# Kernel optimization log

Hardware: AMD Instinct MI355X
Metric: run time of the kernel (lower is better)

Reference implementation:

```python
import jax, jax.numpy as jnp
import numpy as np

HEADS, DH, M_LAND, PINV_ITERS, LN_EPS = 8, 64, 256, 6, 1e-5


def layer_norm(x, g, b):
    mu = x.mean(-1, keepdims=True)
    var = ((x - mu) ** 2).mean(-1, keepdims=True)
    return (x - mu) * jax.lax.rsqrt(var + LN_EPS) * g + b


def moore_penrose_pinv(x, iters=PINV_ITERS):
    # x: (h, m, m). Iterative Newton-Schulz style pinv (lucidrains).
    abs_x = jnp.abs(x)
    col = abs_x.sum(-1)
    row = abs_x.sum(-2)
    z = jnp.swapaxes(x, -1, -2) / (jnp.max(col) * jnp.max(row))
    I = jnp.eye(x.shape[-1], dtype=x.dtype)
    for _ in range(iters):
        xz = x @ z
        z = 0.25 * z @ (13.0 * I - xz @ (15.0 * I - xz @ (7.0 * I - xz)))
    return z


def nystrom_attention(x, qkv_w, out_w, out_b, res_w):
    # x: (n, dim). No mask, eval mode (dropout off).
    n, dim = x.shape
    pad = (-n) % M_LAND
    xp = jnp.pad(x, ((pad, 0), (0, 0)))  # pad at sequence START, as in original
    n_p = n + pad
    l = n_p // M_LAND  # tokens per landmark
    qkv = xp @ qkv_w  # (n_p, 3*h*dh)
    q, k, v = jnp.split(qkv, 3, axis=-1)
    split = lambda t: t.reshape(n_p, HEADS, DH).transpose(1, 0, 2)  # (h, n_p, dh)
    q, k, v = split(q), split(k), split(v)
    q = q * (DH ** -0.5)
    q_l = q.reshape(HEADS, M_LAND, l, DH).mean(axis=2)  # (h, m, dh)
    k_l = k.reshape(HEADS, M_LAND, l, DH).mean(axis=2)
    sim1 = jnp.einsum('hid,hjd->hij', q, k_l)    # (h, n_p, m)
    sim2 = jnp.einsum('hid,hjd->hij', q_l, k_l)  # (h, m, m)
    sim3 = jnp.einsum('hid,hjd->hij', q_l, k)    # (h, m, n_p)
    a1 = jax.nn.softmax(sim1, axis=-1)
    a2 = jax.nn.softmax(sim2, axis=-1)
    a3 = jax.nn.softmax(sim3, axis=-1)
    a2_inv = moore_penrose_pinv(a2)
    out = a1 @ (a2_inv @ (a3 @ v))  # (h, n_p, dh)
    # residual depthwise conv over sequence dim, kernel 33, per head
    res = jax.lax.conv_general_dilated(
        v[None], res_w, (1, 1), ((16, 16), (0, 0)),
        feature_group_count=HEADS, dimension_numbers=('NCHW', 'OIHW', 'NCHW'))[0]
    out = out + res
    out = out.transpose(1, 0, 2).reshape(n_p, HEADS * DH)
    out = out @ out_w + out_b
    return out[-n:]  # drop the leading pad


def ppeg(x, w7, b7, w5, b5, w3, b3, H, W):
    cls_tok, feat = x[0], x[1:]
    C = feat.shape[1]
    img = feat.T.reshape(1, C, H, W)
    def dw(w, b, p):
        y = jax.lax.conv_general_dilated(
            img, w, (1, 1), ((p, p), (p, p)),
            feature_group_count=C, dimension_numbers=('NCHW', 'OIHW', 'NCHW'))
        return y + b.reshape(1, C, 1, 1)
    out = img + dw(w7, b7, 3) + dw(w5, b5, 2) + dw(w3, b3, 1)
    out = out[0].reshape(C, H * W).T
    return jnp.concatenate([cls_tok[None], out], axis=0)


def forward(h, fc1_w, fc1_b, cls_token, l1_ln_g, l1_ln_b, l1_qkv_w, l1_out_w, l1_out_b, l1_res_w,
            conv7_w, conv7_b, conv5_w, conv5_b, conv3_w, conv3_b,
            l2_ln_g, l2_ln_b, l2_qkv_w, l2_out_w, l2_out_b, l2_res_w,
            norm_g, norm_b, fc2_w, fc2_b):
    x = jax.nn.relu(h @ fc1_w + fc1_b)  # (N, 512)
    N = x.shape[0]
    Hs = Ws = int(np.ceil(np.sqrt(N)))  # N chosen perfect square -> add_length == 0
    x = jnp.concatenate([cls_token, x], axis=0)  # (N+1, 512)
    x = x + nystrom_attention(layer_norm(x, l1_ln_g, l1_ln_b), l1_qkv_w, l1_out_w, l1_out_b, l1_res_w)
    x = ppeg(x, conv7_w, conv7_b, conv5_w, conv5_b, conv3_w, conv3_b, Hs, Ws)
    x = x + nystrom_attention(layer_norm(x, l2_ln_g, l2_ln_b), l2_qkv_w, l2_out_w, l2_out_b, l2_res_w)
    x = layer_norm(x, norm_g, norm_b)[0]  # cls token readout
    return x @ fc2_w + fc2_b  # (n_classes,)


def setup_inputs() -> dict:
    key = jax.random.key(0)
    ks = jax.random.split(key, 16)
    nrm = lambda k, s, sc=0.02: jax.random.normal(k, s, jnp.float32) * sc
    D = 512
    return {
        'h': jax.random.normal(ks[0], (16384, 2048), jnp.float32),
        'fc1_w': nrm(ks[1], (2048, D)), 'fc1_b': jnp.zeros((D,), jnp.float32),
        'cls_token': nrm(ks[2], (1, D), 1.0),
        'l1_ln_g': jnp.ones((D,), jnp.float32), 'l1_ln_b': jnp.zeros((D,), jnp.float32),
        'l1_qkv_w': nrm(ks[3], (D, 3 * D)),
        'l1_out_w': nrm(ks[4], (D, D)), 'l1_out_b': jnp.zeros((D,), jnp.float32),
        'l1_res_w': nrm(ks[5], (HEADS, 1, 33, 1), 0.05),
        'conv7_w': nrm(ks[6], (D, 1, 7, 7), 0.05), 'conv7_b': jnp.zeros((D,), jnp.float32),
        'conv5_w': nrm(ks[7], (D, 1, 5, 5), 0.05), 'conv5_b': jnp.zeros((D,), jnp.float32),
        'conv3_w': nrm(ks[8], (D, 1, 3, 3), 0.05), 'conv3_b': jnp.zeros((D,), jnp.float32),
        'l2_ln_g': jnp.ones((D,), jnp.float32), 'l2_ln_b': jnp.zeros((D,), jnp.float32),
        'l2_qkv_w': nrm(ks[9], (D, 3 * D)),
        'l2_out_w': nrm(ks[10], (D, D)), 'l2_out_b': jnp.zeros((D,), jnp.float32),
        'l2_res_w': nrm(ks[11], (HEADS, 1, 33, 1), 0.05),
        'norm_g': jnp.ones((D,), jnp.float32), 'norm_b': jnp.zeros((D,), jnp.float32),
        'fc2_w': nrm(ks[12], (D, 2)), 'fc2_b': jnp.zeros((2,), jnp.float32),
    }


def reference(h, fc1_w, fc1_b, cls_token, l1_ln_g, l1_ln_b, l1_qkv_w, l1_out_w, l1_out_b, l1_res_w,
              conv7_w, conv7_b, conv5_w, conv5_b, conv3_w, conv3_b,
              l2_ln_g, l2_ln_b, l2_qkv_w, l2_out_w, l2_out_b, l2_res_w,
              norm_g, norm_b, fc2_w, fc2_b):
    return forward(h, fc1_w, fc1_b, cls_token, l1_ln_g, l1_ln_b, l1_qkv_w, l1_out_w, l1_out_b, l1_res_w,
                   conv7_w, conv7_b, conv5_w, conv5_b, conv3_w, conv3_b,
                   l2_ln_g, l2_ln_b, l2_qkv_w, l2_out_w, l2_out_b, l2_res_w,
                   norm_g, norm_b, fc2_w, fc2_b)
```

## Files before the change

### kernel.cpp

```cpp
#include <hip/hip_runtime.h>
#include <cstddef>

#define NROWS 16385
#define NPAD  16640
#define PADT  255
#define DIM   512
#define HEADS 8
#define DH    64
#define NL    256
#define LCH   65
#define LCHUNK 65
#define SLACK 24
#define LDST  40
#define AST   72

typedef short bf16x8 __attribute__((ext_vector_type(8)));
typedef float f32x4  __attribute__((ext_vector_type(4)));

__device__ __forceinline__ float wsum(float v){
#pragma unroll
  for (int o = 32; o; o >>= 1) v += __shfl_xor(v, o);
  return v;
}
__device__ __forceinline__ float wmax(float v){
#pragma unroll
  for (int o = 32; o; o >>= 1) v = fmaxf(v, __shfl_xor(v, o));
  return v;
}

__device__ __forceinline__ void split2(float x, unsigned short &h, unsigned short &l){
  unsigned ux = __float_as_uint(x);
  unsigned rh = (ux + 0x7FFFu + ((ux >> 16) & 1u)) >> 16;
  h = (unsigned short)rh;
  float fh = __uint_as_float(rh << 16);
  float r = x - fh;
  unsigned ur = __float_as_uint(r);
  unsigned rl = (ur + 0x7FFFu + ((ur >> 16) & 1u)) >> 16;
  l = (unsigned short)rl;
}
__device__ __forceinline__ float bf2f(unsigned short h){
  return __uint_as_float((unsigned)h << 16);
}

__global__ __launch_bounds__(256) void gemm64_sp_kernel(
    const unsigned short* __restrict__ Ah, const unsigned short* __restrict__ Al,
    const unsigned short* __restrict__ Bth, const unsigned short* __restrict__ Btl,
    const unsigned short* __restrict__ IBh, const unsigned short* __restrict__ IBl,
    float* __restrict__ Cf,
    unsigned short* __restrict__ Crh, unsigned short* __restrict__ Crl,
    unsigned short* __restrict__ Cth, unsigned short* __restrict__ Ctl,
    int M, int N, int K, long sA, long sB, long sC,
    float alpha, float ib)
{
  size_t zo = (size_t)blockIdx.z;
  Ah  += zo*sA; Al  += zo*sA;
  Bth += zo*sB; Btl += zo*sB;
  if (IBh){ IBh += zo*sA; IBl += zo*sA; }
  if (Cf)  Cf  += zo*sC;
  if (Crh){ Crh += zo*sC; Crl += zo*sC; }
  if (Cth){ Cth += zo*sC; Ctl += zo*sC; }
  __shared__ unsigned short LAh[64*LDST], LAl[64*LDST], LBh[64*LDST], LBl[64*LDST];
  const int t = threadIdx.x;
  const int wid = t >> 6, lane = t & 63;
  const int wr = wid >> 1, wc = wid & 1;
  const int l15 = lane & 15, kb = lane >> 4;
  const int bm = blockIdx.y << 6, bn = blockIdx.x << 6;
  const int r4 = t >> 2, kc = (t & 3) << 3;
  f32x4 acc[2][2];
#pragma unroll
  for (int i=0;i<2;++i)
#pragma unroll
    for (int j=0;j<2;++j) acc[i][j] = (f32x4){0.f,0.f,0.f,0.f};

  for (int k0 = 0; k0 < K; k0 += 32){
    __syncthreads();
    {
      int lo = r4*LDST + kc;
      *(uint4*)&LAh[lo] = *(const uint4*)&Ah[(size_t)(bm+r4)*K + k0 + kc];
      *(uint4*)&LAl[lo] = *(const uint4*)&Al[(size_t)(bm+r4)*K + k0 + kc];
      *(uint4*)&LBh[lo] = *(const uint4*)&Bth[(size_t)(bn+r4)*K + k0 + kc];
      *(uint4*)&LBl[lo] = *(const uint4*)&Btl[(size_t)(bn+r4)*K + k0 + kc];
    }
    __syncthreads();
    bf16x8 ah[2], al[2], bh[2], bl[2];
#pragma unroll
    for (int r=0;r<2;++r){
      int off = (wr*32 + r*16 + l15)*LDST + kb*8;
      ah[r] = *(const bf16x8*)&LAh[off];
      al[r] = *(const bf16x8*)&LAl[off];
    }
#pragma unroll
    for (int c2=0;c2<2;++c2){
      int off = (wc*32 + c2*16 + l15)*LDST + kb*8;
      bh[c2] = *(const bf16x8*)&LBh[off];
      bl[c2] = *(const bf16x8*)&LBl[off];
    }
#pragma unroll
    for (int r=0;r<2;++r)
#pragma unroll
      for (int c2=0;c2<2;++c2){
        acc[r][c2] = __builtin_amdgcn_mfma_f32_16x16x32_bf16(ah[r], bh[c2], acc[r][c2], 0,0,0);
        acc[r][c2] = __builtin_amdgcn_mfma_f32_16x16x32_bf16(ah[r], bl[c2], acc[r][c2], 0,0,0);
        acc[r][c2] = __builtin_amdgcn_mfma_f32_16x16x32_bf16(al[r], bh[c2], acc[r][c2], 0,0,0);
      }
  }
#pragma unroll
  for (int r=0;r<2;++r){
#pragma unroll
    for (int c2=0;c2<2;++c2){
      int col = bn + wc*32 + c2*16 + l15;
      int rb  = bm + wr*32 + r*16 + kb*4;
      float v[4];
#pragma unroll
      for (int e=0;e<4;++e){
        float x = acc[r][c2][e];
        if (ib != 0.f){
          size_t io = (size_t)(rb+e)*K + col;
          float ibv = bf2f(IBh[io]) + bf2f(IBl[io]);
          x = alpha*(ib*ibv - x);
        } else {
          x = alpha*x;
        }
        v[e] = x;
      }
      if (Cf){
#pragma unroll
        for (int e=0;e<4;++e) Cf[(size_t)(rb+e)*N + col] = v[e];
      }
      if (Crh){
#pragma unroll
        for (int e=0;e<4;++e){
          unsigned short hh, ll;
          split2(v[e], hh, ll);
          Crh[(size_t)(rb+e)*N + col] = hh;
          Crl[(size_t)(rb+e)*N + col] = ll;
        }
      }
      if (Cth){
        unsigned short h4[4], l4[4];
#pragma unroll
        for (int e=0;e<4;++e) split2(v[e], h4[e], l4[e]);
        uint2 uh, ul;
        uh.x = (unsigned)h4[0] | ((unsigned)h4[1]<<16);
        uh.y = (unsigned)h4[2] | ((unsigned)h4[3]<<16);
        ul.x = (unsigned)l4[0] | ((unsigned)l4[1]<<16);
        ul.y = (unsigned)l4[2] | ((unsigned)l4[3]<<16);
        *(uint2*)&Cth[(size_t)col*M + rb] = uh;
        *(uint2*)&Ctl[(size_t)col*M + rb] = ul;
      }
    }
  }
}

__global__ __launch_bounds__(256) void gemm_sb_kernel(
    const unsigned short* __restrict__ Ah, const unsigned short* __restrict__ Al,
    const unsigned short* __restrict__ BTh, const unsigned short* __restrict__ BTl,
    const float* __restrict__ bias, float* __restrict__ C,
    int M, int N, int K, int accum)
{
  __shared__ unsigned short LAh[128*LDST], LAl[128*LDST], LBh[128*LDST], LBl[128*LDST];
  const int t = threadIdx.x;
  const int bm = blockIdx.y << 7, bn = blockIdx.x << 7;
  const int wid = t >> 6, lane = t & 63;
  const int wr = wid >> 1, wc = wid & 1;
  const int l15 = lane & 15, kb = lane >> 4;
  const int sr = t >> 1, sc0 = (t & 1) << 4;
  f32x4 acc[4][4];
#pragma unroll
  for (int i=0;i<4;++i)
#pragma unroll
    for (int j=0;j<4;++j) acc[i][j] = (f32x4){0.f,0.f,0.f,0.f};

  const uint4 zz = make_uint4(0,0,0,0);
  for (int k0 = 0; k0 < K; k0 += 32){
    __syncthreads();
    {
      bool av = (bm + sr) < M;
      size_t ga = (size_t)(bm + sr)*K + k0 + sc0;
      uint4 a0 = av ? *(const uint4*)(Ah + ga)     : zz;
      uint4 a1 = av ? *(const uint4*)(Ah + ga + 8) : zz;
      uint4 a2 = av ? *(const uint4*)(Al + ga)     : zz;
      uint4 a3 = av ? *(const uint4*)(Al + ga + 8) : zz;
      size_t gb = (size_t)(bn + sr)*K + k0 + sc0;
      uint4 b0 = *(const uint4*)(BTh + gb);
      uint4 b1 = *(const uint4*)(BTh + gb + 8);
      uint4 b2 = *(const uint4*)(BTl + gb);
      uint4 b3 = *(const uint4*)(BTl + gb + 8);
      int lo = sr*LDST + sc0;
      *(uint4*)&LAh[lo] = a0; *(uint4*)&LAh[lo+8] = a1;
      *(uint4*)&LAl[lo] = a2; *(uint4*)&LAl[lo+8] = a3;
      *(uint4*)&LBh[lo] = b0; *(uint4*)&LBh[lo+8] = b1;
      *(uint4*)&LBl[lo] = b2; *(uint4*)&LBl[lo+8] = b3;
    }
    __syncthreads();
    bf16x8 ah[4], al[4], bh[4], bl[4];
#pragma unroll
    for (int ai=0; ai<4; ++ai){
      int off = (wr*64 + ai*16 + l15)*LDST + kb*8;
      ah[ai] = *(const bf16x8*)&LAh[off];
      al[ai] = *(const bf16x8*)&LAl[off];
    }
#pragma unroll
    for (int bj=0; bj<4; ++bj){
      int off = (wc*64 + bj*16 + l15)*LDST + kb*8;
      bh[bj] = *(const bf16x8*)&LBh[off];
      bl[bj] = *(const bf16x8*)&LBl[off];
    }
#pragma unroll
    for (int ai=0; ai<4; ++ai)
#pragma unroll
      for (int bj=0; bj<4; ++bj){
        acc[ai][bj] = __builtin_amdgcn_mfma_f32_16x16x32_bf16(ah[ai], bh[bj], acc[ai][bj], 0,0,0);
        acc[ai][bj] = __builtin_amdgcn_mfma_f32_16x16x32_bf16(ah[ai], bl[bj], acc[ai][bj], 0,0,0);
        acc[ai][bj] = __builtin_amdgcn_mfma_f32_16x16x32_bf16(al[ai], bh[bj], acc[ai][bj], 0,0,0);
      }
  }
#pragma unroll
  for (int ai=0; ai<4; ++ai){
#pragma unroll
    for (int bj=0; bj<4; ++bj){
      int col = bn + wc*64 + bj*16 + l15;
      float bv = bias ? bias[col] : 0.f;
#pragma unroll
      for (int r=0; r<4; ++r){
        int row = bm + wr*64 + ai*16 + kb*4 + r;
        if (row < M){
          float v = acc[ai][bj][r] + bv;
          if (accum) v += C[(size_t)row*N + col];
          C[(size_t)row*N + col] = v;
        }
      }
    }
  }
}

__global__ __launch_bounds__(256) void gemm_sbf_kernel(
    const float* __restrict__ A,
    const unsigned short* __restrict__ BTh, const unsigned short* __restrict__ BTl,
    const float* __restrict__ bias, float* __restrict__ C,
    int M, int N, int K, int relu)
{
  __shared__ unsigned short LAh[128*LDST], LAl[128*LDST], LBh[128*LDST], LBl[128*LDST];
  const int t = threadIdx.x;
  const int bm = blockIdx.y << 7, bn = blockIdx.x << 7;
  const int wid = t >> 6, lane = t & 63;
  const int wr = wid >> 1, wc = wid & 1;
  const int l15 = lane & 15, kb = lane >> 4;
  const int sr = t >> 1, sc0 = (t & 1) << 4;
  f32x4 acc[4][4];
#pragma unroll
  for (int i=0;i<4;++i)
#pragma unroll
    for (int j=0;j<4;++j) acc[i][j] = (f32x4){0.f,0.f,0.f,0.f};

  for (int k0 = 0; k0 < K; k0 += 32){
    __syncthreads();
    {
      const float* ap = A + (size_t)(bm + sr)*K + k0 + sc0;
      float va[16];
      *(float4*)&va[0]  = ((const float4*)ap)[0];
      *(float4*)&va[4]  = ((const float4*)ap)[1];
      *(float4*)&va[8]  = ((const float4*)ap)[2];
      *(float4*)&va[12] = ((const float4*)ap)[3];
      int lo = sr*LDST + sc0;
      unsigned* dh = (unsigned*)&LAh[lo];
      unsigned* dl = (unsigned*)&LAl[lo];
#pragma unroll
      for (int q=0;q<8;++q){
        unsigned short h0,l0,h1,l1;
        split2(va[2*q],   h0, l0);
        split2(va[2*q+1], h1, l1);
        dh[q] = (unsigned)h0 | ((unsigned)h1 << 16);
        dl[q] = (unsigned)l0 | ((unsigned)l1 << 16);
      }
      size_t gb = (size_t)(bn + sr)*K + k0 + sc0;
      uint4 b0 = *(const uint4*)(BTh + gb);
      uint4 b1 = *(const uint4*)(BTh + gb + 8);
      uint4 b2 = *(const uint4*)(BTl + gb);
      uint4 b3 = *(const uint4*)(BTl + gb + 8);
      *(uint4*)&LBh[lo] = b0; *(uint4*)&LBh[lo+8] = b1;
      *(uint4*)&LBl[lo] = b2; *(uint4*)&LBl[lo+8] = b3;
    }
    __syncthreads();
    bf16x8 ah[4], al[4], bh[4], bl[4];
#pragma unroll
    for (int ai=0; ai<4; ++ai){
      int off = (wr*64 + ai*16 + l15)*LDST + kb*8;
      ah[ai] = *(const bf16x8*)&LAh[off];
      al[ai] = *(const bf16x8*)&LAl[off];
    }
#pragma unroll
    for (int bj=0; bj<4; ++bj){
      int off = (wc*64 + bj*16 + l15)*LDST + kb*8;
      bh[bj] = *(const bf16x8*)&LBh[off];
      bl[bj] = *(const bf16x8*)&LBl[off];
    }
#pragma unroll
    for (int ai=0; ai<4; ++ai)
#pragma unroll
      for (int bj=0; bj<4; ++bj){
        acc[ai][bj] = __builtin_amdgcn_mfma_f32_16x16x32_bf16(ah[ai], bh[bj], acc[ai][bj], 0,0,0);
        acc[ai][bj] = __builtin_amdgcn_mfma_f32_16x16x32_bf16(ah[ai], bl[bj], acc[ai][bj], 0,0,0);
        acc[ai][bj] = __builtin_amdgcn_mfma_f32_16x16x32_bf16(al[ai], bh[bj], acc[ai][bj], 0,0,0);
      }
  }
#pragma unroll
  for (int ai=0; ai<4; ++ai){
#pragma unroll
    for (int bj=0; bj<4; ++bj){
      int col = bn + wc*64 + bj*16 + l15;
      float bv = bias ? bias[col] : 0.f;
#pragma unroll
      for (int r=0; r<4; ++r){
        int row = bm + wr*64 + ai*16 + kb*4 + r;
        float v = acc[ai][bj][r] + bv;
        if (relu) v = fmaxf(v, 0.f);
        C[(size_t)row*N + col] = v;
      }
    }
  }
}

__global__ void wt_split_T_kernel(const float* __restrict__ W,
                                  unsigned short* __restrict__ BTh,
                                  unsigned short* __restrict__ BTl, int K, int N)
{
  int idx = blockIdx.x*256 + threadIdx.x;
  if (idx >= N*K) return;
  int n = idx / K, k = idx - n*K;
  unsigned short h, l;
  split2(W[(size_t)k*N + n], h, l);
  BTh[idx] = h; BTl[idx] = l;
}

__global__ void att_split_kernel(const float* __restrict__ ATT,
                                 unsigned short* __restrict__ Ah,
                                 unsigned short* __restrict__ Al)
{
  size_t i4 = (size_t)blockIdx.x*256 + threadIdx.x;
  size_t e = i4*4;
  int row = (int)(e >> 9);
  float4 v = make_float4(0.f,0.f,0.f,0.f);
  if (row < NROWS) v = *(const float4*)(ATT + (size_t)PADT*DIM + e);
  unsigned short h0,l0,h1,l1,h2,l2,h3,l3;
  split2(v.x,h0,l0); split2(v.y,h1,l1); split2(v.z,h2,l2); split2(v.w,h3,l3);
  uint2 uh, ul;
  uh.x = (unsigned)h0 | ((unsigned)h1<<16); uh.y = (unsigned)h2 | ((unsigned)h3<<16);
  ul.x = (unsigned)l0 | ((unsigned)l1<<16); ul.y = (unsigned)l2 | ((unsigned)l3<<16);
  *(uint2*)(Ah + e) = uh;
  *(uint2*)(Al + e) = ul;
}

__global__ __launch_bounds__(256) void ln_pad_sb_kernel(
    const float* __restrict__ X, const float* __restrict__ g,
    const float* __restrict__ b, unsigned short* __restrict__ Yh,
    unsigned short* __restrict__ Yl)
{
  int p = blockIdx.x;
  int t = threadIdx.x;
  size_t base = (size_t)p*DIM;
  if (p < PADT){
    Yh[base+t] = 0; Yh[base+t+256] = 0;
    Yl[base+t] = 0; Yl[base+t+256] = 0;
    return;
  }
  const float* xr = X + (size_t)(p-PADT)*DIM;
  float x0 = xr[t], x1 = xr[t+256];
  float s = x0 + x1, sq = x0*x0 + x1*x1;
  s = wsum(s); sq = wsum(sq);
  __shared__ float rs[4], rq[4];
  if ((t&63)==0){ rs[t>>6]=s; rq[t>>6]=sq; }
  __syncthreads();
  float S = rs[0]+rs[1]+rs[2]+rs[3];
  float SQ = rq[0]+rq[1]+rq[2]+rq[3];
  float mu = S * (1.f/DIM);
  float var = SQ * (1.f/DIM) - mu*mu;
  float r = rsqrtf(var + 1e-5f);
  float y0 = (x0-mu)*r*g[t]     + b[t];
  float y1 = (x1-mu)*r*g[t+256] + b[t+256];
  unsigned short h, l;
  split2(y0, h, l); Yh[base+t] = h;     Yl[base+t] = l;
  split2(y1, h, l); Yh[base+t+256] = h; Yl[base+t+256] = l;
}

__global__ void landmarks_kernel(const float* __restrict__ QKV,
                                 float* __restrict__ QL, float* __restrict__ KL)
{
  int m = blockIdx.x, h = blockIdx.y, d = threadIdx.x;
  float sq = 0.f, sk = 0.f;
  const float* base = QKV + (size_t)(m*LCH)*1536 + (h<<6) + d;
  for (int j = 0; j < LCH; ++j){
    sq += base[0];
    sk += base[512];
    base += 1536;
  }
  QL[(((h<<8)+m)<<6) + d] = sq * (0.125f/65.f);
  KL[(((h<<8)+m)<<6) + d] = sk * (1.f/65.f);
}

__global__ void klsplit_kernel(const float* __restrict__ KL,
                               unsigned short* __restrict__ KLh,
                               unsigned short* __restrict__ KLl)
{
  int i = blockIdx.x*256 + threadIdx.x;
  unsigned short h, l;
  split2(KL[i], h, l);
  KLh[i] = h; KLl[i] = l;
}

__global__ __launch_bounds__(256) void sim2_kernel(
    const float* __restrict__ QL, const float* __restrict__ KL, float* __restrict__ A2)
{
  int m = blockIdx.x, h = blockIdx.y, n = threadIdx.x;
  __shared__ float ql[64];
  __shared__ float red[4];
  if (n < 64) ql[n] = QL[(((h<<8)+m)<<6) + n];
  __syncthreads();
  const float* kl = KL + (size_t)(((h<<8)+n)<<6);
  float s = 0.f;
#pragma unroll
  for (int d=0; d<64; ++d) s += ql[d]*kl[d];
  float mx = wmax(s);
  if ((n&63)==0) red[n>>6] = mx;
  __syncthreads();
  mx = fmaxf(fmaxf(red[0],red[1]), fmaxf(red[2],red[3]));
  float e = __expf(s - mx);
  float sm = wsum(e);
  __syncthreads();
  if ((n&63)==0) red[n>>6] = sm;
  __syncthreads();
  sm = red[0]+red[1]+red[2]+red[3];
  A2[((size_t)((h<<8)+m)<<8) + n] = e/sm;
}

__global__ void crsum_kernel(const float* __restrict__ A2, float* __restrict__ CR)
{
  int b = blockIdx.x, t = threadIdx.x;
  float v;
  if (b < 2048){
    v = fabsf(A2[((size_t)b<<8) + t]);
  } else {
    int r = b - 2048;
    int h = r >> 8, n = r & 255;
    v = fabsf(A2[((size_t)h<<16) + (t<<8) + n]);
  }
  v = wsum(v);
  __shared__ float red[4];
  if ((t&63)==0) red[t>>6]=v;
  __syncthreads();
  if (t==0) CR[b] = red[0]+red[1]+red[2]+red[3];
}
__global__ void maxprod_kernel(const float* __restrict__ CR, float* __restrict__ SCAL)
{
  int t = threadIdx.x;
  float mc = -3e38f, mr = -3e38f;
  for (int i=t; i<2048; i+=256){ mc = fmaxf(mc, CR[i]); mr = fmaxf(mr, CR[2048+i]); }
  mc = wmax(mc); mr = wmax(mr);
  __shared__ float rc[4], rr[4];
  if ((t&63)==0){ rc[t>>6]=mc; rr[t>>6]=mr; }
  __syncthreads();
  if (t==0){
    float a = fmaxf(fmaxf(rc[0],rc[1]),fmaxf(rc[2],rc[3]));
    float b = fmaxf(fmaxf(rr[0],rr[1]),fmaxf(rr[2],rr[3]));
    SCAL[0] = 1.f/(a*b);
  }
}

__global__ void tsplit_kernel(const float* __restrict__ A2, const float* __restrict__ SCAL,
                              unsigned short* __restrict__ A2h, unsigned short* __restrict__ A2l,
                              unsigned short* __restrict__ Zrh, unsigned short* __restrict__ Zrl,
                              unsigned short* __restrict__ Zth, unsigned short* __restrict__ Ztl)
{
  int idx = blockIdx.x*256 + threadIdx.x;
  int h = idx >> 16, rem = idx & 65535, m = rem >> 8, n = rem & 255;
  float a = A2[idx];
  unsigned short hh, ll;
  split2(a, hh, ll);
  A2h[idx] = hh; A2l[idx] = ll;
  float z = a * SCAL[0];
  split2(z, hh, ll);
  Zth[idx] = hh; Ztl[idx] = ll;
  size_t rmo = ((size_t)h<<16) + (n<<8) + m;
  Zrh[rmo] = hh; Zrl[rmo] = ll;
}

__global__ __launch_bounds__(256) void lattn3_kernel(
    const float* __restrict__ QKV, const float* __restrict__ QL,
    float* __restrict__ PACC, float* __restrict__ PML)
{
  const int c = blockIdx.x, lg = blockIdx.y, h = blockIdx.z;
  const int t = threadIdx.x;
  const int w = t >> 6, lane = t & 63;
  const int l15 = lane & 15, kb = lane >> 4;
  __shared__ unsigned short LQh[64*AST], LQl[64*AST];
  __shared__ unsigned short LKh[64*AST], LKl[64*AST];
  __shared__ unsigned short LPh[64*AST], LPl[64*AST];
  const int sr = t >> 2, sc0 = (t & 3) << 4;
  {
    const float* qp = QL + (((size_t)(h*256 + lg*64 + sr)) << 6) + sc0;
    float va[16];
    *(float4*)&va[0]  = ((const float4*)qp)[0];
    *(float4*)&va[4]  = ((const float4*)qp)[1];
    *(float4*)&va[8]  = ((const float4*)qp)[2];
    *(float4*)&va[12] = ((const float4*)qp)[3];
    unsigned* dh = (unsigned*)&LQh[sr*AST + sc0];
    unsigned* dl = (unsigned*)&LQl[sr*AST + sc0];
#pragma unroll
    for (int q=0;q<8;++q){
      unsigned short h0,l0,h1,l1;
      split2(va[2*q],   h0, l0);
      split2(va[2*q+1], h1, l1);
      dh[q] = (unsigned)h0 | ((unsigned)h1 << 16);
      dl[q] = (unsigned)l0 | ((unsigned)l1 << 16);
    }
  }
  float m = -3e38f, l = 0.f;
  f32x4 oacc[4];
#pragma unroll
  for (int i=0;i<4;++i) oacc[i] = (f32x4){0.f,0.f,0.f,0.f};

  for (int s = 0; s < 4; ++s){
    const int kbase = c*256 + s*64;
    __syncthreads();
    {
      const float* kp = QKV + (size_t)(kbase + sr)*1536 + 512 + (h<<6) + sc0;
      float va[16];
      *(float4*)&va[0]  = ((const float4*)kp)[0];
      *(float4*)&va[4]  = ((const float4*)kp)[1];
      *(float4*)&va[8]  = ((const float4*)kp)[2];
      *(float4*)&va[12] = ((const float4*)kp)[3];
      unsigned* dh = (unsigned*)&LKh[sr*AST + sc0];
      unsigned* dl = (unsigned*)&LKl[sr*AST + sc0];
#pragma unroll
      for (int q=0;q<8;++q){
        unsigned short h0,l0,h1,l1;
        split2(va[2*q],   h0, l0);
        split2(va[2*q+1], h1, l1);
        dh[q] = (unsigned)h0 | ((unsigned)h1 << 16);
        dl[q] = (unsigned)l0 | ((unsigned)l1 << 16);
      }
    }
    __syncthreads();
    f32x4 sacc[4];
#pragma unroll
    for (int i=0;i<4;++i) sacc[i] = (f32x4){0.f,0.f,0.f,0.f};
#pragma unroll
    for (int ks = 0; ks < 2; ++ks){
      int qoff = (w*16 + l15)*AST + ks*32 + kb*8;
      bf16x8 bh = *(const bf16x8*)&LQh[qoff];
      bf16x8 bl = *(const bf16x8*)&LQl[qoff];
#pragma unroll
      for (int mi=0; mi<4; ++mi){
        int aoff = (mi*16 + l15)*AST + ks*32 + kb*8;
        bf16x8 ah = *(const bf16x8*)&LKh[aoff];
        bf16x8 al = *(const bf16x8*)&LKl[aoff];
        sacc[mi] = __builtin_amdgcn_mfma_f32_16x16x32_bf16(ah, bh, sacc[mi], 0,0,0);
        sacc[mi] = __builtin_amdgcn_mfma_f32_16x16x32_bf16(ah, bl, sacc[mi], 0,0,0);
        sacc[mi] = __builtin_amdgcn_mfma_f32_16x16x32_bf16(al, bh, sacc[mi], 0,0,0);
      }
    }
// ... 270 lines not shown
{
  int i = blockIdx.x*256 + threadIdx.x;
  QKV[(size_t)NPAD*1536 + i] = 0.f;
}

__global__ __launch_bounds__(256) void convres2_kernel(
    const float* __restrict__ QKV, const float* __restrict__ rw,
    float* __restrict__ ATT)
{
  const int t = threadIdx.x;
  const int c = blockIdx.y*256 + t;
  const int i0 = PADT + (blockIdx.x << 2);
  const int h = c >> 6;
  float w[33];
#pragma unroll
  for (int k=0;k<33;++k) w[k] = rw[h*33 + k];
  float acc[4] = {0.f,0.f,0.f,0.f};
  const float* vbase = QKV + (size_t)(i0-16)*1536 + 1024 + c;
#pragma unroll
  for (int rr=0; rr<36; ++rr){
    float v = vbase[(size_t)rr*1536];
#pragma unroll
    for (int k=0;k<4;++k){
      int tap = rr - k;
      if (tap >= 0 && tap <= 32) acc[k] += w[tap]*v;
    }
  }
#pragma unroll
  for (int k=0;k<4;++k){
    int i = i0 + k;
    if (i < NPAD) ATT[(size_t)i*DIM + c] += acc[k];
  }
}

__global__ void pad_kernel(const float* __restrict__ X, float* __restrict__ PIM)
{
  int r = blockIdx.x;
  int c = blockIdx.y*256 + threadIdx.x;
  int py = r / 134, px = r - py*134;
  float v = 0.f;
  if (py>=3 && py<131 && px>=3 && px<131)
    v = X[(size_t)(1 + (py-3)*128 + (px-3))*512 + c];
  PIM[(size_t)r*512 + c] = v;
}

__global__ void wtrans_kernel(const float* __restrict__ w7, const float* __restrict__ w5,
                              const float* __restrict__ w3, float* __restrict__ W7T,
                              float* __restrict__ W5T, float* __restrict__ W3T)
{
  int i = blockIdx.x;
  int c = blockIdx.y*256 + threadIdx.x;
  if (i < 49)      W7T[i*512+c]      = w7[c*49+i];
  else if (i < 74) W5T[(i-49)*512+c] = w5[c*25+(i-49)];
  else             W3T[(i-74)*512+c] = w3[c*9+(i-74)];
}

__global__ __launch_bounds__(256) void ppeg2_kernel(
    const float* __restrict__ PIM, const float* __restrict__ W7T,
    const float* __restrict__ W5T, const float* __restrict__ W3T,
    const float* __restrict__ b7, const float* __restrict__ b5,
    const float* __restrict__ b3, float* __restrict__ X2)
{
  const int t = threadIdx.x;
  const int c = blockIdx.z*256 + t;
  const int x = blockIdx.x;
  const int y0 = blockIdx.y << 2;
  float w7r[49], w5r[25], w3r[9];
#pragma unroll
  for (int i=0;i<49;++i) w7r[i] = W7T[i*512 + c];
#pragma unroll
  for (int i=0;i<25;++i) w5r[i] = W5T[i*512 + c];
#pragma unroll
  for (int i=0;i<9;++i)  w3r[i] = W3T[i*512 + c];
  const float bsum = b7[c] + b5[c] + b3[c];
  float acc[4] = {bsum, bsum, bsum, bsum};
  const float* base = PIM + ((size_t)(y0*134 + x))*512 + c;
#pragma unroll
  for (int rr=0; rr<10; ++rr){
#pragma unroll
    for (int cc=0; cc<7; ++cc){
      float v = base[(size_t)(rr*134 + cc)*512];
#pragma unroll
      for (int k=0;k<4;++k){
        const int dy = rr - k - 3, dx = cc - 3;
        if (dy >= -3 && dy <= 3){
          acc[k] += w7r[(dy+3)*7 + (dx+3)] * v;
          if (dy >= -2 && dy <= 2 && dx >= -2 && dx <= 2)
            acc[k] += w5r[(dy+2)*5 + (dx+2)] * v;
          if (dy >= -1 && dy <= 1 && dx >= -1 && dx <= 1)
            acc[k] += w3r[(dy+1)*3 + (dx+1)] * v;
          if (dy == 0 && dx == 0) acc[k] += v;
        }
      }
    }
  }
#pragma unroll
  for (int k=0;k<4;++k)
    X2[(size_t)(1 + (y0+k)*128 + x)*512 + c] = acc[k];
}

__global__ void copy_row_kernel(const float* __restrict__ src, float* __restrict__ dst)
{
  dst[threadIdx.x] = src[threadIdx.x];
}

__global__ void final_kernel(const float* __restrict__ X, const float* __restrict__ g,
                             const float* __restrict__ b, const float* __restrict__ fw,
                             const float* __restrict__ fb, float* __restrict__ out)
{
  int t = threadIdx.x;
  float x0 = X[t], x1 = X[t+256];
  float s = x0 + x1, sq = x0*x0 + x1*x1;
  s = wsum(s); sq = wsum(sq);
  __shared__ float rs[4], rq[4];
  if ((t&63)==0){ rs[t>>6]=s; rq[t>>6]=sq; }
  __syncthreads();
  float S = rs[0]+rs[1]+rs[2]+rs[3];
  float SQ = rq[0]+rq[1]+rq[2]+rq[3];
  float mu = S*(1.f/DIM);
  float var = SQ*(1.f/DIM) - mu*mu;
  float r = rsqrtf(var + 1e-5f);
  float n0 = (x0-mu)*r*g[t]     + b[t];
  float n1 = (x1-mu)*r*g[t+256] + b[t+256];
  float p0 = n0*fw[t*2]   + n1*fw[(t+256)*2];
  float p1 = n0*fw[t*2+1] + n1*fw[(t+256)*2+1];
  p0 = wsum(p0); p1 = wsum(p1);
  __shared__ float r0[4], r1[4];
  if ((t&63)==0){ r0[t>>6]=p0; r1[t>>6]=p1; }
  __syncthreads();
  if (t==0){
    out[0] = r0[0]+r0[1]+r0[2]+r0[3] + fb[0];
    out[1] = r1[0]+r1[1]+r1[2]+r1[3] + fb[1];
  }
}

struct Bufs {
  float *Y, *QKV, *QL, *KL, *A2, *CR, *SCAL, *PACC, *PML, *W7T, *W5T, *W3T;
  unsigned short *Yh, *Yl, *ATh, *ATl, *qBTh, *qBTl, *oBTh, *oBTl, *fBTh, *fBTl;
  unsigned short *A2h, *A2l, *XZrh, *XZrl, *XZth, *XZtl, *Wth, *Wtl, *W2th, *W2tl;
  unsigned short *Z0rh, *Z0rl, *Z0th, *Z0tl, *Z1rh, *Z1rl, *Z1th, *Z1tl;
  unsigned short *TMth, *TMtl, *KLh, *KLl, *BMth, *BMtl;
};

static void attention_layer(float* X, const float* ln_g, const float* ln_b,
                            const float* qkv_w, const float* out_w, const float* out_b,
                            const float* res_w, Bufs& bf, hipStream_t stream)
{
  const long SP = 65536;
  wt_split_T_kernel<<<(1536*512)/256, 256, 0, stream>>>(qkv_w, bf.qBTh, bf.qBTl, 512, 1536);
  wt_split_T_kernel<<<(512*512)/256, 256, 0, stream>>>(out_w, bf.oBTh, bf.oBTl, 512, 512);
  ln_pad_sb_kernel<<<NPAD, 256, 0, stream>>>(X, ln_g, ln_b, bf.Yh, bf.Yl);
  gemm_sb_kernel<<<dim3(12,130),256,0,stream>>>(bf.Yh, bf.Yl, bf.qBTh, bf.qBTl,
      nullptr, bf.QKV, NPAD, 1536, 512, 0);
  landmarks_kernel<<<dim3(NL,HEADS),64,0,stream>>>(bf.QKV, bf.QL, bf.KL);
  klsplit_kernel<<<512,256,0,stream>>>(bf.KL, bf.KLh, bf.KLl);
  sim2_kernel<<<dim3(NL,HEADS),256,0,stream>>>(bf.QL, bf.KL, bf.A2);
  crsum_kernel<<<4096,256,0,stream>>>(bf.A2, bf.CR);
  maxprod_kernel<<<1,256,0,stream>>>(bf.CR, bf.SCAL);
  tsplit_kernel<<<2048,256,0,stream>>>(bf.A2, bf.SCAL, bf.A2h, bf.A2l,
      bf.Z0rh, bf.Z0rl, bf.Z0th, bf.Z0tl);
  unsigned short *Zarh=bf.Z0rh, *Zarl=bf.Z0rl, *Zath=bf.Z0th, *Zatl=bf.Z0tl;
  unsigned short *Zbrh=bf.Z1rh, *Zbrl=bf.Z1rl, *Zbth=bf.Z1th, *Zbtl=bf.Z1tl;
  for (int it = 0; it < 6; ++it){
    gemm64_sp_kernel<<<dim3(4,4,8),256,0,stream>>>(bf.A2h, bf.A2l, Zath, Zatl,
        nullptr, nullptr, nullptr, bf.XZrh, bf.XZrl, bf.XZth, bf.XZtl,
        256,256,256, SP,SP,SP, 1.f, 0.f);
    gemm64_sp_kernel<<<dim3(4,4,8),256,0,stream>>>(bf.XZrh, bf.XZrl, bf.XZth, bf.XZtl,
        bf.XZrh, bf.XZrl, nullptr, nullptr, nullptr, bf.Wth, bf.Wtl,
        256,256,256, SP,SP,SP, 1.f, 7.f);
    gemm64_sp_kernel<<<dim3(4,4,8),256,0,stream>>>(bf.XZrh, bf.XZrl, bf.Wth, bf.Wtl,
        bf.XZrh, bf.XZrl, nullptr, nullptr, nullptr, bf.W2th, bf.W2tl,
        256,256,256, SP,SP,SP, 1.f, 15.f);
    gemm64_sp_kernel<<<dim3(4,4,8),256,0,stream>>>(Zarh, Zarl, bf.W2th, bf.W2tl,
        Zarh, Zarl, nullptr, Zbrh, Zbrl, Zbth, Zbtl,
        256,256,256, SP,SP,SP, 0.25f, 13.f);
    unsigned short* tp;
    tp=Zarh; Zarh=Zbrh; Zbrh=tp;  tp=Zarl; Zarl=Zbrl; Zbrl=tp;
    tp=Zath; Zath=Zbth; Zbth=tp;  tp=Zatl; Zatl=Zbtl; Zbtl=tp;
  }
  lattn3_kernel<<<dim3(LCHUNK,4,HEADS),256,0,stream>>>(bf.QKV, bf.QL, bf.PACC, bf.PML);
  lattn_combine_kernel<<<2048,64,0,stream>>>(bf.PACC, bf.PML, bf.TMth, bf.TMtl);
  gemm64_sp_kernel<<<dim3(1,4,8),256,0,stream>>>(Zarh, Zarl, bf.TMth, bf.TMtl,
      nullptr, nullptr, nullptr, nullptr, nullptr, bf.BMth, bf.BMtl,
      256,64,256, SP, 16384L, 16384L, 1.f, 0.f);
  float* ATT = bf.Y;
  attn3_kernel<<<dim3(257,HEADS),256,0,stream>>>(bf.QKV, bf.KLh, bf.KLl,
      bf.BMth, bf.BMtl, ATT);
  convres2_kernel<<<dim3(4097,2),256,0,stream>>>(bf.QKV, res_w, ATT);
  att_split_kernel<<<8256,256,0,stream>>>(ATT, bf.ATh, bf.ATl);
  gemm_sb_kernel<<<dim3(4,129),256,0,stream>>>(bf.ATh, bf.ATl, bf.oBTh, bf.oBTl,
      out_b, X, NROWS, 512, 512, 1);
}

extern "C" void kernel_launch(void* const* d_in, const int* in_sizes, int n_in,
                              void* d_out, int out_size, void* d_ws, size_t ws_size,
                              hipStream_t stream)
{
  (void)in_sizes; (void)n_in; (void)out_size; (void)ws_size;
  const float* h       = (const float*)d_in[0];
  const float* fc1_w   = (const float*)d_in[1];
  const float* fc1_b   = (const float*)d_in[2];
  const float* cls     = (const float*)d_in[3];
  const float* l1_ln_g = (const float*)d_in[4];
  const float* l1_ln_b = (const float*)d_in[5];
  const float* l1_qkv_w= (const float*)d_in[6];
  const float* l1_out_w= (const float*)d_in[7];
  const float* l1_out_b= (const float*)d_in[8];
  const float* l1_res_w= (const float*)d_in[9];
  const float* conv7_w = (const float*)d_in[10];
  const float* conv7_b = (const float*)d_in[11];
  const float* conv5_w = (const float*)d_in[12];
  const float* conv5_b = (const float*)d_in[13];
  const float* conv3_w = (const float*)d_in[14];
  const float* conv3_b = (const float*)d_in[15];
  const float* l2_ln_g = (const float*)d_in[16];
  const float* l2_ln_b = (const float*)d_in[17];
  const float* l2_qkv_w= (const float*)d_in[18];
  const float* l2_out_w= (const float*)d_in[19];
  const float* l2_out_b= (const float*)d_in[20];
  const float* l2_res_w= (const float*)d_in[21];
  const float* norm_g  = (const float*)d_in[22];
  const float* norm_b  = (const float*)d_in[23];
  const float* fc2_w   = (const float*)d_in[24];
  const float* fc2_b   = (const float*)d_in[25];

  float* ws = (float*)d_ws;
  float* X   = ws;                 ws += (size_t)NROWS*DIM;
  float* X2  = ws;                 ws += (size_t)NROWS*DIM;
  Bufs bf;
  bf.Y    = ws;                    ws += (size_t)NPAD*DIM;
  bf.QKV  = ws;                    ws += (size_t)(NPAD+SLACK)*1536;
  bf.QL   = ws;                    ws += HEADS*NL*DH;
  bf.KL   = ws;                    ws += HEADS*NL*DH;
  bf.A2   = ws;                    ws += HEADS*NL*NL;
  bf.CR   = ws;                    ws += 4096;
  bf.SCAL = ws;                    ws += 8;
  bf.PACC = ws;                    ws += (size_t)LCHUNK*HEADS*NL*DH;
  bf.PML  = ws;                    ws += (size_t)LCHUNK*HEADS*NL*2;
  bf.W7T  = ws;                    ws += 49*512;
  bf.W5T  = ws;                    ws += 25*512;
  bf.W3T  = ws;                    ws += 9*512;
  unsigned short* us = (unsigned short*)ws;
  bf.Yh   = us;                    us += (size_t)NPAD*DIM;
  bf.Yl   = us;                    us += (size_t)NPAD*DIM;
  bf.ATh  = us;                    us += (size_t)16512*DIM;
  bf.ATl  = us;                    us += (size_t)16512*DIM;
  bf.qBTh = us;                    us += 1536*512;
  bf.qBTl = us;                    us += 1536*512;
  bf.oBTh = us;                    us += 512*512;
  bf.oBTl = us;                    us += 512*512;
  bf.fBTh = us;                    us += 512*2048;
  bf.fBTl = us;                    us += 512*2048;
  const size_t PL = (size_t)HEADS*NL*NL;
  bf.A2h  = us; us += PL;  bf.A2l  = us; us += PL;
  bf.XZrh = us; us += PL;  bf.XZrl = us; us += PL;
  bf.XZth = us; us += PL;  bf.XZtl = us; us += PL;
  bf.Wth  = us; us += PL;  bf.Wtl  = us; us += PL;
  bf.W2th = us; us += PL;  bf.W2tl = us; us += PL;
  bf.Z0rh = us; us += PL;  bf.Z0rl = us; us += PL;
  bf.Z0th = us; us += PL;  bf.Z0tl = us; us += PL;
  bf.Z1rh = us; us += PL;  bf.Z1rl = us; us += PL;
  bf.Z1th = us; us += PL;  bf.Z1tl = us; us += PL;
  bf.TMth = us; us += (size_t)HEADS*NL*DH;
  bf.TMtl = us; us += (size_t)HEADS*NL*DH;
  bf.KLh  = us; us += (size_t)HEADS*NL*DH;
  bf.KLl  = us; us += (size_t)HEADS*NL*DH;
  bf.BMth = us; us += (size_t)HEADS*NL*DH;
  bf.BMtl = us; us += (size_t)HEADS*NL*DH;
  float* PIM = bf.QKV;

  zero_slack_kernel<<<(SLACK*1536)/256, 256, 0, stream>>>(bf.QKV);
  wtrans_kernel<<<dim3(83,2),256,0,stream>>>(conv7_w, conv5_w, conv3_w,
                                             bf.W7T, bf.W5T, bf.W3T);

  wt_split_T_kernel<<<(512*2048)/256, 256, 0, stream>>>(fc1_w, bf.fBTh, bf.fBTl, 2048, 512);
  gemm_sbf_kernel<<<dim3(4,128),256,0,stream>>>(h, bf.fBTh, bf.fBTl, fc1_b, X + DIM,
      16384, 512, 2048, 1);
  copy_row_kernel<<<1,512,0,stream>>>(cls, X);

  attention_layer(X, l1_ln_g, l1_ln_b, l1_qkv_w, l1_out_w, l1_out_b, l1_res_w, bf, stream);

  pad_kernel<<<dim3(17956,2),256,0,stream>>>(X, PIM);
  ppeg2_kernel<<<dim3(128,32,2),256,0,stream>>>(PIM, bf.W7T, bf.W5T, bf.W3T,
                                                conv7_b, conv5_b, conv3_b, X2);
  copy_row_kernel<<<1,512,0,stream>>>(X, X2);

  attention_layer(X2, l2_ln_g, l2_ln_b, l2_qkv_w, l2_out_w, l2_out_b, l2_res_w, bf, stream);

  final_kernel<<<1,256,0,stream>>>(X2, norm_g, norm_b, fc2_w, fc2_b, (float*)d_out);
}
```

Before: 1.943 ms.

## Split-K the fc1 GEMM, fuse pinv polynomial GEMMs, fold KL split into landmarks

The fc1 GEMM (16384x512x2048) now runs split-K over two z-slices into a scratch buffer, and a new elementwise kernel adds the two partials, the bias and the ReLU. This raises the block count from 512 to 1024 so more CUs are busy, at the cost of writing and re-reading a 2x16384x512 partial buffer. The Newton-Schulz pinv step is algebraically regrouped: xz^2 is computed once and 13I-15xz+7xz^2-xz^3 is formed in one GEMM epilogue that takes two extra input operands and a diagonal term, so each iteration keeps four GEMMs but no longer needs the separate 7I and 15I epilogues. The klsplit kernel is merged into landmarks_kernel, removing one launch.

```diff
diff --git a/kernel.cpp b/kernel.cpp
--- a/kernel.cpp
+++ b/kernel.cpp
@@ -45,17 +45,19 @@
 __global__ __launch_bounds__(256) void gemm64_sp_kernel(
     const unsigned short* __restrict__ Ah, const unsigned short* __restrict__ Al,
     const unsigned short* __restrict__ Bth, const unsigned short* __restrict__ Btl,
-    const unsigned short* __restrict__ IBh, const unsigned short* __restrict__ IBl,
+    const unsigned short* __restrict__ IB1h, const unsigned short* __restrict__ IB1l,
+    const unsigned short* __restrict__ IB2h, const unsigned short* __restrict__ IB2l,
     float* __restrict__ Cf,
     unsigned short* __restrict__ Crh, unsigned short* __restrict__ Crl,
     unsigned short* __restrict__ Cth, unsigned short* __restrict__ Ctl,
     int M, int N, int K, long sA, long sB, long sC,
-    float alpha, float ib)
+    float aAcc, float cDiag, float c1, float c2)
 {
   size_t zo = (size_t)blockIdx.z;
   Ah  += zo*sA; Al  += zo*sA;
   Bth += zo*sB; Btl += zo*sB;
-  if (IBh){ IBh += zo*sA; IBl += zo*sA; }
+  if (IB1h){ IB1h += zo*sA; IB1l += zo*sA; }
+  if (IB2h){ IB2h += zo*sA; IB2l += zo*sA; }
   if (Cf)  Cf  += zo*sC;
   if (Crh){ Crh += zo*sC; Crl += zo*sC; }
   if (Cth){ Cth += zo*sC; Ctl += zo*sC; }
@@ -90,36 +92,39 @@
       al[r] = *(const bf16x8*)&LAl[off];
     }
 #pragma unroll
-    for (int c2=0;c2<2;++c2){
-      int off = (wc*32 + c2*16 + l15)*LDST + kb*8;
-      bh[c2] = *(const bf16x8*)&LBh[off];
-      bl[c2] = *(const bf16x8*)&LBl[off];
+    for (int c2v=0;c2v<2;++c2v){
+      int off = (wc*32 + c2v*16 + l15)*LDST + kb*8;
+      bh[c2v] = *(const bf16x8*)&LBh[off];
+      bl[c2v] = *(const bf16x8*)&LBl[off];
     }
 #pragma unroll
     for (int r=0;r<2;++r)
 #pragma unroll
-      for (int c2=0;c2<2;++c2){
-        acc[r][c2] = __builtin_amdgcn_mfma_f32_16x16x32_bf16(ah[r], bh[c2], acc[r][c2], 0,0,0);
-        acc[r][c2] = __builtin_amdgcn_mfma_f32_16x16x32_bf16(ah[r], bl[c2], acc[r][c2], 0,0,0);
-        acc[r][c2] = __builtin_amdgcn_mfma_f32_16x16x32_bf16(al[r], bh[c2], acc[r][c2], 0,0,0);
+      for (int c2v=0;c2v<2;++c2v){
+        acc[r][c2v] = __builtin_amdgcn_mfma_f32_16x16x32_bf16(ah[r], bh[c2v], acc[r][c2v], 0,0,0);
+        acc[r][c2v] = __builtin_amdgcn_mfma_f32_16x16x32_bf16(ah[r], bl[c2v], acc[r][c2v], 0,0,0);
+        acc[r][c2v] = __builtin_amdgcn_mfma_f32_16x16x32_bf16(al[r], bh[c2v], acc[r][c2v], 0,0,0);
       }
   }
 #pragma unroll
   for (int r=0;r<2;++r){
 #pragma unroll
-    for (int c2=0;c2<2;++c2){
-      int col = bn + wc*32 + c2*16 + l15;
+    for (int c2v=0;c2v<2;++c2v){
+      int col = bn + wc*32 + c2v*16 + l15;
       int rb  = bm + wr*32 + r*16 + kb*4;
       float v[4];
 #pragma unroll
       for (int e=0;e<4;++e){
-        float x = acc[r][c2][e];
-        if (ib != 0.f){
-          size_t io = (size_t)(rb+e)*K + col;
-          float ibv = bf2f(IBh[io]) + bf2f(IBl[io]);
-          x = alpha*(ib*ibv - x);
-        } else {
-          x = alpha*x;
+        float x = aAcc*acc[r][c2v][e];
+        int row = rb + e;
+        if (cDiag != 0.f && row == col) x += cDiag;
+        if (IB1h){
+          size_t io = (size_t)row*K + col;
+          x += c1*(bf2f(IB1h[io]) + bf2f(IB1l[io]));
+        }
+        if (IB2h){
+          size_t io = (size_t)row*K + col;
+          x += c2*(bf2f(IB2h[io]) + bf2f(IB2l[io]));
         }
         v[e] = x;
       }
@@ -238,8 +243,11 @@
     const float* __restrict__ A,
     const unsigned short* __restrict__ BTh, const unsigned short* __restrict__ BTl,
     const float* __restrict__ bias, float* __restrict__ C,
-    int M, int N, int K, int relu)
-{
+    int M, int N, int K, int relu, int ksplit)
+{
+  const int kLen = K / ksplit;
+  const int kOff = blockIdx.z * kLen;
+  if (ksplit > 1) C += (size_t)blockIdx.z * M * N;
   __shared__ unsigned short LAh[128*LDST], LAl[128*LDST], LBh[128*LDST], LBl[128*LDST];
   const int t = threadIdx.x;
   const int bm = blockIdx.y << 7, bn = blockIdx.x << 7;
@@ -253,7 +261,7 @@
 #pragma unroll
     for (int j=0;j<4;++j) acc[i][j] = (f32x4){0.f,0.f,0.f,0.f};
 
-  for (int k0 = 0; k0 < K; k0 += 32){
+  for (int k0 = kOff; k0 < kOff + kLen; k0 += 32){
     __syncthreads();
     {
       const float* ap = A + (size_t)(bm + sr)*K + k0 + sc0;
@@ -309,16 +317,31 @@
 #pragma unroll
     for (int bj=0; bj<4; ++bj){
       int col = bn + wc*64 + bj*16 + l15;
-      float bv = bias ? bias[col] : 0.f;
+      float bv = (bias && ksplit==1) ? bias[col] : 0.f;
 #pragma unroll
       for (int r=0; r<4; ++r){
         int row = bm + wr*64 + ai*16 + kb*4 + r;
         float v = acc[ai][bj][r] + bv;
-        if (relu) v = fmaxf(v, 0.f);
+        if (relu && ksplit==1) v = fmaxf(v, 0.f);
         C[(size_t)row*N + col] = v;
       }
     }
   }
+}
+
+__global__ void fc1fix_kernel(const float* __restrict__ CP, const float* __restrict__ bias,
+                              float* __restrict__ X)
+{
+  size_t i = (size_t)blockIdx.x*256 + threadIdx.x;
+  float4 a = ((const float4*)CP)[i];
+  float4 b = ((const float4*)CP)[i + 2097152];
+  float4 bb = ((const float4*)bias)[i & 127];
+  float4 o;
+  o.x = fmaxf(a.x + b.x + bb.x, 0.f);
+  o.y = fmaxf(a.y + b.y + bb.y, 0.f);
+  o.z = fmaxf(a.z + b.z + bb.z, 0.f);
+  o.w = fmaxf(a.w + b.w + bb.w, 0.f);
+  ((float4*)X)[i] = o;
 }
 
 __global__ void wt_split_T_kernel(const float* __restrict__ W,
@@ -384,7 +407,9 @@
 }
 
 __global__ void landmarks_kernel(const float* __restrict__ QKV,
-                                 float* __restrict__ QL, float* __restrict__ KL)
+                                 float* __restrict__ QL, float* __restrict__ KL,
+                                 unsigned short* __restrict__ KLh,
+                                 unsigned short* __restrict__ KLl)
 {
   int m = blockIdx.x, h = blockIdx.y, d = threadIdx.x;
   float sq = 0.f, sk = 0.f;
@@ -394,18 +419,13 @@
     sk += base[512];
     base += 1536;
   }
-  QL[(((h<<8)+m)<<6) + d] = sq * (0.125f/65.f);
-  KL[(((h<<8)+m)<<6) + d] = sk * (1.f/65.f);
-}
-
-__global__ void klsplit_kernel(const float* __restrict__ KL,
-                               unsigned short* __restrict__ KLh,
-                               unsigned short* __restrict__ KLl)
-{
-  int i = blockIdx.x*256 + threadIdx.x;
-  unsigned short h, l;
-  split2(KL[i], h, l);
-  KLh[i] = h; KLl[i] = l;
+  size_t off = (((size_t)(h<<8)+m)<<6) + d;
+  float klv = sk * (1.f/65.f);
+  QL[off] = sq * (0.125f/65.f);
+  KL[off] = klv;
+  unsigned short hh, ll;
+  split2(klv, hh, ll);
+  KLh[off] = hh; KLl[off] = ll;
 }
 
 __global__ __launch_bounds__(256) void sim2_kernel(
@@ -982,8 +1002,7 @@
   ln_pad_sb_kernel<<<NPAD, 256, 0, stream>>>(X, ln_g, ln_b, bf.Yh, bf.Yl);
   gemm_sb_kernel<<<dim3(12,130),256,0,stream>>>(bf.Yh, bf.Yl, bf.qBTh, bf.qBTl,
       nullptr, bf.QKV, NPAD, 1536, 512, 0);
-  landmarks_kernel<<<dim3(NL,HEADS),64,0,stream>>>(bf.QKV, bf.QL, bf.KL);
-  klsplit_kernel<<<512,256,0,stream>>>(bf.KL, bf.KLh, bf.KLl);
+  landmarks_kernel<<<dim3(NL,HEADS),64,0,stream>>>(bf.QKV, bf.QL, bf.KL, bf.KLh, bf.KLl);
   sim2_kernel<<<dim3(NL,HEADS),256,0,stream>>>(bf.QL, bf.KL, bf.A2);
   crsum_kernel<<<4096,256,0,stream>>>(bf.A2, bf.CR);
   maxprod_kernel<<<1,256,0,stream>>>(bf.CR, bf.SCAL);
@@ -993,17 +1012,21 @@
   unsigned short *Zbrh=bf.Z1rh, *Zbrl=bf.Z1rl, *Zbth=bf.Z1th, *Zbtl=bf.Z1tl;
   for (int it = 0; it < 6; ++it){
     gemm64_sp_kernel<<<dim3(4,4,8),256,0,stream>>>(bf.A2h, bf.A2l, Zath, Zatl,
-        nullptr, nullptr, nullptr, bf.XZrh, bf.XZrl, bf.XZth, bf.XZtl,
-        256,256,256, SP,SP,SP, 1.f, 0.f);
+        nullptr,nullptr, nullptr,nullptr, nullptr,
+        bf.XZrh, bf.XZrl, bf.XZth, bf.XZtl,
+        256,256,256, SP,SP,SP, 1.f, 0.f, 0.f, 0.f);
     gemm64_sp_kernel<<<dim3(4,4,8),256,0,stream>>>(bf.XZrh, bf.XZrl, bf.XZth, bf.XZtl,
-        bf.XZrh, bf.XZrl, nullptr, nullptr, nullptr, bf.Wth, bf.Wtl,
-        256,256,256, SP,SP,SP, 1.f, 7.f);
-    gemm64_sp_kernel<<<dim3(4,4,8),256,0,stream>>>(bf.XZrh, bf.XZrl, bf.Wth, bf.Wtl,
-        bf.XZrh, bf.XZrl, nullptr, nullptr, nullptr, bf.W2th, bf.W2tl,
-        256,256,256, SP,SP,SP, 1.f, 15.f);
-    gemm64_sp_kernel<<<dim3(4,4,8),256,0,stream>>>(Zarh, Zarl, bf.W2th, bf.W2tl,
-        Zarh, Zarl, nullptr, Zbrh, Zbrl, Zbth, Zbtl,
-        256,256,256, SP,SP,SP, 0.25f, 13.f);
+        nullptr,nullptr, nullptr,nullptr, nullptr,
+        bf.Wth, bf.Wtl, bf.W2th, bf.W2tl,
+        256,256,256, SP,SP,SP, 1.f, 0.f, 0.f, 0.f);
+    gemm64_sp_kernel<<<dim3(4,4,8),256,0,stream>>>(bf.XZrh, bf.XZrl, bf.W2th, bf.W2tl,
+        bf.XZrh, bf.XZrl, bf.Wth, bf.Wtl, nullptr,
+        nullptr, nullptr, bf.XZth, bf.XZtl,
+        256,256,256, SP,SP,SP, -1.f, 13.f, -15.f, 7.f);
+    gemm64_sp_kernel<<<dim3(4,4,8),256,0,stream>>>(Zarh, Zarl, bf.XZth, bf.XZtl,
+        nullptr,nullptr, nullptr,nullptr, nullptr,
+        Zbrh, Zbrl, Zbth, Zbtl,
+        256,256,256, SP,SP,SP, 0.25f, 0.f, 0.f, 0.f);
     unsigned short* tp;
     tp=Zarh; Zarh=Zbrh; Zbrh=tp;  tp=Zarl; Zarl=Zbrl; Zbrl=tp;
     tp=Zath; Zath=Zbth; Zbth=tp;  tp=Zatl; Zatl=Zbtl; Zbtl=tp;
@@ -1011,8 +1034,9 @@
   lattn3_kernel<<<dim3(LCHUNK,4,HEADS),256,0,stream>>>(bf.QKV, bf.QL, bf.PACC, bf.PML);
   lattn_combine_kernel<<<2048,64,0,stream>>>(bf.PACC, bf.PML, bf.TMth, bf.TMtl);
   gemm64_sp_kernel<<<dim3(1,4,8),256,0,stream>>>(Zarh, Zarl, bf.TMth, bf.TMtl,
-      nullptr, nullptr, nullptr, nullptr, nullptr, bf.BMth, bf.BMtl,
-      256,64,256, SP, 16384L, 16384L, 1.f, 0.f);
+      nullptr,nullptr, nullptr,nullptr, nullptr,
+      nullptr, nullptr, bf.BMth, bf.BMtl,
+      256,64,256, SP, 16384L, 16384L, 1.f, 0.f, 0.f, 0.f);
   float* ATT = bf.Y;
   attn3_kernel<<<dim3(257,HEADS),256,0,stream>>>(bf.QKV, bf.KLh, bf.KLl,
       bf.BMth, bf.BMtl, ATT);
@@ -1098,14 +1122,16 @@
   bf.BMth = us; us += (size_t)HEADS*NL*DH;
   bf.BMtl = us; us += (size_t)HEADS*NL*DH;
   float* PIM = bf.QKV;
+  float* CP  = bf.Y;
 
   zero_slack_kernel<<<(SLACK*1536)/256, 256, 0, stream>>>(bf.QKV);
   wtrans_kernel<<<dim3(83,2),256,0,stream>>>(conv7_w, conv5_w, conv3_w,
                                              bf.W7T, bf.W5T, bf.W3T);
 
   wt_split_T_kernel<<<(512*2048)/256, 256, 0, stream>>>(fc1_w, bf.fBTh, bf.fBTl, 2048, 512);
-  gemm_sbf_kernel<<<dim3(4,128),256,0,stream>>>(h, bf.fBTh, bf.fBTl, fc1_b, X + DIM,
-      16384, 512, 2048, 1);
+  gemm_sbf_kernel<<<dim3(4,128,2),256,0,stream>>>(h, bf.fBTh, bf.fBTl, nullptr, CP,
+      16384, 512, 2048, 0, 2);
+  fc1fix_kernel<<<8192,256,0,stream>>>(CP, fc1_b, X + DIM);
   copy_row_kernel<<<1,512,0,stream>>>(cls, X);
 
   attention_layer(X, l1_ln_g, l1_ln_b, l1_qkv_w, l1_out_w, l1_out_b, l1_res_w, bf, stream);
```

New measurement: 2.006 ms. 3.2% more time.
